# Optimization experiments

Measured on AMD Instinct MI355X. Metric: run time of the kernel, lower is better.

The kernel has to match this reference:

```python
import jax, jax.numpy as jnp
import numpy as np

B, L, D, H = 1, 2048, 1024, 16
d = D // H  # head dim = 64


def setup_inputs() -> dict:
    key = jax.random.key(0)
    ks = jax.random.split(key, 8)
    s = 1.0 / np.sqrt(D)
    return {
        "x": jax.random.normal(ks[0], (B, L, D), jnp.float32),
        "Wqkv_w": (jax.random.normal(ks[1], (D, 3 * D), jnp.float32) * s),
        "Wqkv_b": jnp.zeros((3 * D,), jnp.float32),
        "out_w": (jax.random.normal(ks[2], (D, D), jnp.float32) * s),
        "out_b": jnp.zeros((D,), jnp.float32),
        "W_static": jnp.zeros((H, d, d), jnp.float32),
        "Lambda_raw": jax.random.uniform(ks[3], (H, d, d), jnp.float32, -3.0, 3.0),
        "Gamma": jax.random.uniform(ks[4], (H, d, d), jnp.float32, -0.5 / np.sqrt(d), 0.5 / np.sqrt(d)),
        "gate_w1": (jax.random.normal(ks[5], (D, D // 2), jnp.float32) * s),
        "gate_b1": jnp.zeros((D // 2,), jnp.float32),
        "gate_w2": (jax.random.normal(ks[6], (D // 2, H), jnp.float32) * (1.0 / np.sqrt(D // 2))),
        "gate_b2": jnp.zeros((H,), jnp.float32),
    }


def _forward(x, Wqkv_w, Wqkv_b, out_w, out_b, W_static, Lambda_raw, Gamma,
             gate_w1, gate_b1, gate_w2, gate_b2):
    Bb, Ll, Dm = x.shape
    Hh = Gamma.shape[0]
    dd = Dm // Hh
    scale = 1.0 / np.sqrt(dd)

    # qkv projection: (B,L,3D) -> (3, B, H, L, d) layout
    qkv = (x @ Wqkv_w + Wqkv_b).reshape(Bb, Ll, 3, Hh, dd)
    q = jnp.transpose(qkv[:, :, 0], (0, 2, 1, 3))  # (B,H,L,d)
    k = jnp.transpose(qkv[:, :, 1], (0, 2, 1, 3))
    v = jnp.transpose(qkv[:, :, 2], (0, 2, 1, 3))

    # --- softmax branch (causal, additive -10000 mask like the original) ---
    scores = jnp.einsum('bhid,bhjd->bhij', q, k) * scale
    causal_mask = jnp.triu(jnp.full((Ll, Ll), -10000.0, dtype=scores.dtype), 1)
    attn = jax.nn.softmax(scores + causal_mask, axis=-1)
    y_softmax = jnp.einsum('bhij,bhjd->bhid', attn, v)

    # --- STP branch: linear recurrence over time via lax.scan ---
    retention = 1.0 - jax.nn.sigmoid(Lambda_raw)  # (H,d,d)
    k_stp = k * scale

    def step(state, inp):
        q_t, k_t, v_t = inp  # each (B,H,d)
        hebbian = v_t[..., :, None] * k_t[..., None, :]          # (B,H,d,d)
        state = retention * state + Gamma * hebbian              # (B,H,d,d)
        y_t = jnp.einsum('bhij,bhj->bhi', W_static + state, q_t)  # (B,H,d)
        return state, y_t

    state0 = jnp.zeros((Bb, Hh, dd, dd), x.dtype)
    qT = jnp.moveaxis(q, 2, 0)      # (L,B,H,d)
    kT = jnp.moveaxis(k_stp, 2, 0)
    vT = jnp.moveaxis(v, 2, 0)
    _, ys = jax.lax.scan(step, state0, (qT, kT, vT))
    y_stp = jnp.moveaxis(ys, 0, 2)  # (B,H,L,d)

    # --- learned gate: Linear -> GELU(exact) -> Linear -> sigmoid ---
    g = jax.nn.gelu(x @ gate_w1 + gate_b1, approximate=False)
    alpha = jax.nn.sigmoid(g @ gate_w2 + gate_b2)        # (B,L,H)
    alpha = jnp.transpose(alpha, (0, 2, 1))[..., None]   # (B,H,L,1)

    y = alpha * y_softmax + (1.0 - alpha) * y_stp        # (B,H,L,d)
    y = jnp.transpose(y, (0, 2, 1, 3)).reshape(Bb, Ll, Dm)
    return y @ out_w + out_b


def reference(x, Wqkv_w, Wqkv_b, out_w, out_b, W_static, Lambda_raw, Gamma,
              gate_w1, gate_b1, gate_w2, gate_b2):
    return _forward(x, Wqkv_w, Wqkv_b, out_w, out_b, W_static, Lambda_raw,
                    Gamma, gate_w1, gate_b1, gate_w2, gate_b2)
```

## Files before the change

### kernel.cpp

```cpp
#include <hip/hip_runtime.h>
#include <hip/hip_bf16.h>

#define L_SEQ 2048
#define DMODEL 1024
#define NHEAD 16
#define DHEAD 64
#define D3 3072

typedef __attribute__((ext_vector_type(8))) short s8v;
typedef __attribute__((ext_vector_type(4))) float f4v;
typedef unsigned int u32;
#define AS1 __attribute__((address_space(1)))
#define AS3 __attribute__((address_space(3)))

__device__ __forceinline__ short f2bf(float f) {
  __hip_bfloat16 h = __float2bfloat16(f);
  return *reinterpret_cast<short*>(&h);
}
__device__ __forceinline__ float bf2f(short s) {
  return __uint_as_float(((u32)(unsigned short)s) << 16);
}
__device__ __forceinline__ int pack2bf(float lo, float hi) {
  return (int)(((unsigned)(unsigned short)f2bf(hi) << 16) |
               (unsigned)(unsigned short)f2bf(lo));
}

__device__ __forceinline__ void transpose32(const float* __restrict__ W,
    short* __restrict__ Wt, int K, int N, int bx, int by, int tid)
{
  __shared__ float T[32][33];
  int col = tid & 31, rb = tid >> 5;
  #pragma unroll
  for (int it = 0; it < 4; ++it) {
    int r = it * 8 + rb;
    T[r][col] = W[(size_t)(by * 32 + r) * N + bx * 32 + col];
  }
  __syncthreads();
  #pragma unroll
  for (int it = 0; it < 4; ++it) {
    int r = it * 8 + rb;
    Wt[(size_t)(bx * 32 + r) * K + by * 32 + col] = f2bf(T[col][r]);
  }
}

__global__ __launch_bounds__(256) void prep_kernel(
    const float* __restrict__ x, short* __restrict__ xb,
    const float* __restrict__ Wqkv_w, const float* __restrict__ gw1,
    const float* __restrict__ out_w, short* __restrict__ wt_buf,
    short* __restrict__ wtO)
{
  int b = blockIdx.x, tid = threadIdx.x;
  if (b < 2048) {
    int i = (b * 256 + tid) * 4;
    float4 v = *(const float4*)(x + i);
    short4 o;
    o.x = f2bf(v.x); o.y = f2bf(v.y); o.z = f2bf(v.z); o.w = f2bf(v.w);
    *(short4*)(xb + i) = o;
  } else if (b < 5120) {
    int r = b - 2048;
    transpose32(Wqkv_w, wt_buf, 1024, 3072, r % 96, r / 96, tid);
  } else if (b < 5632) {
    int r = b - 5120;
    transpose32(gw1, wt_buf + 3072 * 1024, 1024, 512, r % 16, r / 16, tid);
  } else {
    int r = b - 5632;
    transpose32(out_w, wtO, 1024, 1024, r % 32, r / 32, tid);
  }
}

template<int BM, int BN, int MODE>
__global__ __launch_bounds__(256, 6) void gemm_mfma(
    const short* __restrict__ A, const short* __restrict__ Bt,
    const float* __restrict__ bias, const float* __restrict__ bias2,
    float* __restrict__ C, short* __restrict__ C2,
    short* __restrict__ QbP, short* __restrict__ KbP,
    int M, int N, int K)
{
  constexpr int LA = BM / 64, LB = BN / 64;
  constexpr int WM = BM / 2, WN = BN / 2;
  constexpr int MT = WM / 16, NT = WN / 16;
  __shared__ __align__(16) short As[2][BM * 32];
  __shared__ __align__(16) short Bs[2][BN * 32];
  const int tid = threadIdx.x;
  const int w = tid >> 6, lane = tid & 63;
  const int quad = lane >> 4, c = lane & 15;
  int n0, kb, ke;
  size_t cofs = 0;
  if (MODE == 3) {
    n0 = (blockIdx.x & 15) * BN;
    int kh = blockIdx.x >> 4;
    kb = kh * (K / 2); ke = kb + K / 2;
    cofs = (size_t)kh * M * N;
  } else {
    n0 = blockIdx.x * BN; kb = 0; ke = K;
  }
  const int m0 = blockIdx.y * BM;
  const int wm = (w & 1) * WM, wn = (w >> 1) * WN;
  f4v acc[MT][NT] = {};

  auto stage = [&](int buf, int k0) {
    #pragma unroll
    for (int it = 0; it < LA; ++it) {
      int off = (it * 256 + tid) * 16;
      int row = off >> 6, colh = (off & 63) >> 1;
      __builtin_amdgcn_global_load_lds(
          (const AS1 u32*)(A + (size_t)(m0 + row) * K + k0 + colh),
          (AS3 u32*)(&As[buf][0] + (off >> 1)), 16, 0, 0);
    }
    #pragma unroll
    for (int it = 0; it < LB; ++it) {
      int off = (it * 256 + tid) * 16;
      int row = off >> 6, colh = (off & 63) >> 1;
      __builtin_amdgcn_global_load_lds(
          (const AS1 u32*)(Bt + (size_t)(n0 + row) * K + k0 + colh),
          (AS3 u32*)(&Bs[buf][0] + (off >> 1)), 16, 0, 0);
    }
  };
  stage(0, kb);
  int cur = 0;
  for (int k0 = kb; k0 < ke; k0 += 32) {
    __syncthreads();
    if (k0 + 32 < ke) stage(cur ^ 1, k0 + 32);
    s8v af[MT], bf[NT];
    #pragma unroll
    for (int mt = 0; mt < MT; ++mt)
      af[mt] = *(s8v*)&As[cur][(wm + mt * 16 + c) * 32 + quad * 8];
    #pragma unroll
    for (int nt = 0; nt < NT; ++nt)
      bf[nt] = *(s8v*)&Bs[cur][(wn + nt * 16 + c) * 32 + quad * 8];
    #pragma unroll
    for (int mt = 0; mt < MT; ++mt)
      #pragma unroll
      for (int nt = 0; nt < NT; ++nt)
        acc[mt][nt] = __builtin_amdgcn_mfma_f32_16x16x32_bf16(
            af[mt], bf[nt], acc[mt][nt], 0, 0, 0);
    cur ^= 1;
  }
  #pragma unroll
  for (int mt = 0; mt < MT; ++mt)
    #pragma unroll
    for (int r = 0; r < 4; ++r) {
      int m = m0 + wm + mt * 16 + quad * 4 + r;
      #pragma unroll
      for (int nt = 0; nt < NT; ++nt) {
        int n = n0 + wn + nt * 16 + c;
        float v = acc[mt][nt][r];
        if (MODE == 3) {
          C[cofs + (size_t)m * N + n] = v;
        } else {
          if (n < 2048) {
            float v2 = v + bias[n];
            int hh = (n >> 6) & 15, ee = n & 63;
            short* dst = (n < 1024) ? QbP : KbP;
            dst[((size_t)hh * 2048 + m) * 64 + ee] = f2bf(v2);
          } else if (n < 3072) {
            C[(size_t)m * 1024 + (n - 2048)] = v + bias[n];
          } else {
            float t = v + bias2[n - 3072];
            t = 0.5f * t * (1.0f + erff(t * 0.70710678118654752f));
            C2[(size_t)m * 512 + (n - 3072)] = f2bf(t);
          }
        }
      }
    }
}

__global__ __launch_bounds__(256) void splitk_add(const float* __restrict__ Cp,
    const float* __restrict__ bias, float* __restrict__ out)
{
  int i = (blockIdx.x * 256 + threadIdx.x) * 4;
  float4 a = *(const float4*)(Cp + i);
  float4 b = *(const float4*)(Cp + 2097152 + i);
  float4 bs = *(const float4*)(bias + (i & 1023));
  float4 o;
  o.x = a.x + b.x + bs.x; o.y = a.y + b.y + bs.y;
  o.z = a.z + b.z + bs.z; o.w = a.w + b.w + bs.w;
  *(float4*)(out + i) = o;
}

__device__ __forceinline__ int piece_slot(int qt, int h, int p) {
  if (qt >= 16) return (qt - 16) * 48 + h * 3 + p;
  if (qt >= 8)  return 768 + (qt - 8) * 32 + h * 2 + p;
  return 1024 + qt * 16 + h;
}

__global__ __launch_bounds__(256) void attn_mfma(
    const short* __restrict__ Qb, const short* __restrict__ Kb,
    const short* __restrict__ Vtb, float* __restrict__ Opart,
    float* __restrict__ mpart, float* __restrict__ lpart)
{
  const int bid = blockIdx.x;
  int h, qt, p, np;
  if (bid < 768)       { int j = bid;        qt = 31 - j / 48; int r = j % 48; h = r / 3; p = r % 3; np = 3; }
  else if (bid < 1024) { int j = bid - 768;  qt = 15 - j / 32; int r = j % 32; h = r >> 1; p = r & 1; np = 2; }
  else                 { int j = bid - 1024; qt = 7 - (j >> 4); h = j & 15; p = 0; np = 1; }
  const int n = qt + 1;
  const int ts = (p * n) / np, te = ((p + 1) * n) / np;
  const int ps = piece_slot(qt, h, p);
  float* Odst = Opart + (size_t)ps * 4096;
  float* mdst = mpart + ps * 64;
  float* ldst = lpart + ps * 64;

  const int q0 = qt * 64;
  const int tid = threadIdx.x;
  const int w = tid >> 6, lane = tid & 63;
  const int quad = lane >> 4, c = lane & 15;

  __shared__ __align__(16) char smem[27648];
  short* Ks = (short*)smem;
  short* Vt = Ks + 4608;
  short* Ps = Vt + 4608;
  float* Ob = (float*)smem;

  const int qrow = q0 + w * 16 + c;
  s8v qf[2];
  qf[0] = *(const s8v*)(Qb + ((size_t)h * 2048 + qrow) * 64 + quad * 8);
  qf[1] = *(const s8v*)(Qb + ((size_t)h * 2048 + qrow) * 64 + 32 + quad * 8);

  const int srow = tid >> 3, sc = (tid & 7) * 8;
  int4 pk0, pk1, pv0, pv1;
  auto load_tile = [&](int t0) {
    const short* kbase = Kb + ((size_t)h * 2048 + t0 * 64) * 64;
    const short* vbase = Vtb + (size_t)h * 64 * 2048 + t0 * 64;
    pk0 = *(const int4*)(kbase + (size_t)srow * 64 + sc);
    pk1 = *(const int4*)(kbase + (size_t)(srow + 32) * 64 + sc);
    pv0 = *(const int4*)(vbase + (size_t)srow * 2048 + sc);
    pv1 = *(const int4*)(vbase + (size_t)(srow + 32) * 2048 + sc);
  };
  load_tile(ts);

  f4v o_acc[4] = {};
  float m = -1e30f, l = 0.f;

  for (int t0 = ts; t0 < te; ++t0) {
    __syncthreads();
    *(int4*)&Ks[srow * 72 + sc] = pk0;
    *(int4*)&Ks[(srow + 32) * 72 + sc] = pk1;
    *(int4*)&Vt[srow * 72 + sc] = pv0;
    *(int4*)&Vt[(srow + 32) * 72 + sc] = pv1;
    __syncthreads();
    if (t0 + 1 < te) load_tile(t0 + 1);

    f4v s_acc[4] = {};
    #pragma unroll
    for (int kt = 0; kt < 4; ++kt) {
      #pragma unroll
      for (int kc = 0; kc < 2; ++kc) {
        s8v kf = *(s8v*)&Ks[(kt * 16 + c) * 72 + kc * 32 + quad * 8];
        s_acc[kt] = __builtin_amdgcn_mfma_f32_16x16x32_bf16(kf, qf[kc], s_acc[kt], 0, 0, 0);
      }
    }
    float sv[4][4];
    bool full = (t0 * 64 + 63) <= (q0 + w * 16);
    #pragma unroll
    for (int kt = 0; kt < 4; ++kt)
      #pragma unroll
      for (int r = 0; r < 4; ++r) {
        float s = s_acc[kt][r] * 0.125f;
        if (!full) {
          int key = t0 * 64 + kt * 16 + quad * 4 + r;
          s = (key <= qrow) ? s : -1e30f;
        }
        sv[kt][r] = s;
      }
    float mloc = -1e30f;
    #pragma unroll
    for (int kt = 0; kt < 4; ++kt)
      #pragma unroll
      for (int r = 0; r < 4; ++r) mloc = fmaxf(mloc, sv[kt][r]);
    mloc = fmaxf(mloc, __shfl_xor(mloc, 16));
    mloc = fmaxf(mloc, __shfl_xor(mloc, 32));
    float mnew = fmaxf(fmaxf(m, mloc), -1e20f);
    float alpha = __expf(m - mnew);
    m = mnew;
    float pv[4][4], ls = 0.f;
    #pragma unroll
    for (int kt = 0; kt < 4; ++kt)
      #pragma unroll
      for (int r = 0; r < 4; ++r) { pv[kt][r] = __expf(sv[kt][r] - mnew); ls += pv[kt][r]; }
    ls += __shfl_xor(ls, 16);
    ls += __shfl_xor(ls, 32);
    l = l * alpha + ls;
    #pragma unroll
    for (int mt = 0; mt < 4; ++mt)
      #pragma unroll
      for (int r = 0; r < 4; ++r) o_acc[mt][r] *= alpha;
    short* Pw = Ps + w * 1152;
    #pragma unroll
    for (int kt = 0; kt < 4; ++kt) {
      *(int*)&Pw[c * 72 + kt * 16 + quad * 4]     = pack2bf(pv[kt][0], pv[kt][1]);
      *(int*)&Pw[c * 72 + kt * 16 + quad * 4 + 2] = pack2bf(pv[kt][2], pv[kt][3]);
    }
    #pragma unroll
    for (int kc2 = 0; kc2 < 2; ++kc2) {
      s8v pf = *(s8v*)&Pw[c * 72 + kc2 * 32 + quad * 8];
      #pragma unroll
      for (int mt = 0; mt < 4; ++mt) {
        s8v vf = *(s8v*)&Vt[(mt * 16 + c) * 72 + kc2 * 32 + quad * 8];
        o_acc[mt] = __builtin_amdgcn_mfma_f32_16x16x32_bf16(vf, pf, o_acc[mt], 0, 0, 0);
      }
    }
  }

  __syncthreads();
  #pragma unroll
  for (int mt = 0; mt < 4; ++mt)
    #pragma unroll
    for (int r = 0; r < 4; ++r)
      Ob[(w * 16 + c) * 66 + mt * 16 + quad * 4 + r] = o_acc[mt][r];
  if (quad == 0) { mdst[w * 16 + c] = m; ldst[w * 16 + c] = l; }
  __syncthreads();
  for (int i = tid; i < 4096; i += 256)
    Odst[i] = Ob[(i >> 6) * 66 + (i & 63)];
}

__global__ __launch_bounds__(256) void attn_merge(
    const float* __restrict__ Opart, const float* __restrict__ mpart,
    const float* __restrict__ lpart, const float* __restrict__ ystp,
    const float* __restrict__ alpha, short* __restrict__ ycb)
{
  int bid = blockIdx.x;
  int h = bid >> 5, qt = bid & 31;
  int np = (qt >= 16) ? 3 : ((qt >= 8) ? 2 : 1);
  int ps0 = piece_slot(qt, h, 0);
  int tid = threadIdx.x;
  for (int it = 0; it < 16; ++it) {
    int idx = it * 256 + tid;
    int q = idx >> 6, e = idx & 63;
    int gq = qt * 64 + q;
    float ms = mpart[ps0 * 64 + q];
    for (int p2 = 1; p2 < np; ++p2)
      ms = fmaxf(ms, mpart[(ps0 + p2) * 64 + q]);
    float oo = 0.f, ll = 0.f;
    for (int p2 = 0; p2 < np; ++p2) {
      float wp = __expf(mpart[(ps0 + p2) * 64 + q] - ms);
      oo += Opart[(size_t)(ps0 + p2) * 4096 + idx] * wp;
      ll += lpart[(ps0 + p2) * 64 + q] * wp;
    }
    float ys = oo / ll;
    float a = alpha[gq * 16 + h];
    float yst = ystp[((size_t)h * 2048 + gq) * 64 + e];
    ycb[(size_t)gq * 1024 + h * 64 + e] = f2bf(a * ys + (1.f - a) * yst);
  }
}

__global__ __launch_bounds__(256) void stp_local(const float* __restrict__ Vf,
    const short* __restrict__ Kb, const float* __restrict__ Lam,
    const float* __restrict__ Gam, float* __restrict__ states,
    short* __restrict__ Vtb)
{
  int c = blockIdx.x, h = blockIdx.y;
  int tid = threadIdx.x;
  int i = tid >> 2, j0 = (tid & 3) * 16;
  __shared__ float Kc[64][64];
  __shared__ float Vc[64][65];
  for (int idx = tid; idx < 1024; idx += 256) {
    int t = idx >> 4, e4 = (idx & 15) * 4;
    short4 ks = *(const short4*)(Kb + ((size_t)h * 2048 + c * 64 + t) * 64 + e4);
    Kc[t][e4]     = bf2f(ks.x) * 0.125f;
    Kc[t][e4 + 1] = bf2f(ks.y) * 0.125f;
    Kc[t][e4 + 2] = bf2f(ks.z) * 0.125f;
    Kc[t][e4 + 3] = bf2f(ks.w) * 0.125f;
    float4 vv = *(const float4*)(Vf + (size_t)(c * 64 + t) * 1024 + h * 64 + e4);
    Vc[t][e4] = vv.x; Vc[t][e4 + 1] = vv.y; Vc[t][e4 + 2] = vv.z; Vc[t][e4 + 3] = vv.w;
  }
  float r[16], g[16], s[16];
  #pragma unroll
  for (int e = 0; e < 16; ++e) {
    int idx = h * 4096 + i * 64 + j0 + e;
    r[e] = 1.f / (1.f + expf(Lam[idx]));
    g[e] = Gam[idx];
    s[e] = 0.f;
  }
  __syncthreads();
  for (int idx = tid; idx < 2048; idx += 256) {
    int dim = idx >> 5, k2 = idx & 31;
    *(int*)&Vtb[((size_t)h * 64 + dim) * 2048 + c * 64 + k2 * 2] =
        pack2bf(Vc[k2 * 2][dim], Vc[k2 * 2 + 1][dim]);
  }
  for (int t = 0; t < 64; ++t) {
    float v = Vc[t][i];
    #pragma unroll
    for (int e = 0; e < 16; ++e)
      s[e] = r[e] * s[e] + g[e] * (v * Kc[t][j0 + e]);
  }
  #pragma unroll
  for (int e = 0; e < 16; ++e)
    states[((size_t)h * 32 + c) * 4096 + i * 64 + j0 + e] = s[e];
}

__global__ __launch_bounds__(256) void stp_scan(const float* __restrict__ Lam,
                                                float* __restrict__ states)
{
  int gid = blockIdx.x * 256 + threadIdx.x;
  float r = 1.f / (1.f + expf(Lam[gid]));
  float r64 = r;
  #pragma unroll
  for (int q = 0; q < 6; ++q) r64 *= r64;
  int h = gid >> 12, low = gid & 4095;
  const size_t base = (size_t)h * 32 * 4096 + low;
  float v[32];
  #pragma unroll
  for (int c = 0; c < 32; ++c) v[c] = states[base + (size_t)c * 4096];
  float acc = 0.f;
  #pragma unroll
  for (int c = 0; c < 32; ++c) {
    float d = v[c];
    v[c] = acc;
    acc = r64 * acc + d;
  }
  #pragma unroll
  for (int c = 0; c < 32; ++c) states[base + (size_t)c * 4096] = v[c];
}

__global__ __launch_bounds__(256) void stp_out(const float* __restrict__ Vf,
    const short* __restrict__ Kb, const short* __restrict__ Qb,
    const float* __restrict__ Lam, const float* __restrict__ Gam,
    const float* __restrict__ Wst, const float* __restrict__ states,
    float* __restrict__ ystp)
{
  int c = blockIdx.x, h = blockIdx.y;
  int tid = threadIdx.x;
  int i = tid >> 2, j0 = (tid & 3) * 16;
  __shared__ float Kc[64][64];
  __shared__ float Vc[64][64];
  __shared__ float Qc[64][64];
  for (int idx = tid; idx < 1024; idx += 256) {
    int t = idx >> 4, e4 = (idx & 15) * 4;
    size_t bo = ((size_t)h * 2048 + c * 64 + t) * 64 + e4;
    short4 ks = *(const short4*)(Kb + bo);
    short4 qs = *(const short4*)(Qb + bo);
    Kc[t][e4]     = bf2f(ks.x) * 0.125f;
    Kc[t][e4 + 1] = bf2f(ks.y) * 0.125f;
    Kc[t][e4 + 2] = bf2f(ks.z) * 0.125f;
    Kc[t][e4 + 3] = bf2f(ks.w) * 0.125f;
    Qc[t][e4]     = bf2f(qs.x);
    Qc[t][e4 + 1] = bf2f(qs.y);
    Qc[t][e4 + 2] = bf2f(qs.z);
    Qc[t][e4 + 3] = bf2f(qs.w);
    float4 vv = *(const float4*)(Vf + (size_t)(c * 64 + t) * 1024 + h * 64 + e4);
    Vc[t][e4] = vv.x; Vc[t][e4 + 1] = vv.y; Vc[t][e4 + 2] = vv.z; Vc[t][e4 + 3] = vv.w;
  }
  float r[16], g[16], s[16], w[16];
  #pragma unroll
  for (int e = 0; e < 16; ++e) {
    int idx = h * 4096 + i * 64 + j0 + e;
    r[e] = 1.f / (1.f + expf(Lam[idx]));
    g[e] = Gam[idx];
    w[e] = Wst[idx];
    s[e] = states[((size_t)h * 32 + c) * 4096 + i * 64 + j0 + e];
  }
  __syncthreads();
  for (int t = 0; t < 64; ++t) {
    float v = Vc[t][i];
    float y = 0.f;
    #pragma unroll
    for (int e = 0; e < 16; ++e) {
      s[e] = r[e] * s[e] + g[e] * (v * Kc[t][j0 + e]);
      y += (w[e] + s[e]) * Qc[t][j0 + e];
    }
    y += __shfl_xor(y, 1);
    y += __shfl_xor(y, 2);
    if ((tid & 3) == 0)
      ystp[((size_t)h * L_SEQ + c * 64 + t) * 64 + i] = y;
  }
}

__global__ __launch_bounds__(256) void gate2_kernel(const short* __restrict__ g_bf,
    const float* __restrict__ w2, const float* __restrict__ b2,
    float* __restrict__ alpha)
{
  int tid = threadIdx.x;
  int gid = blockIdx.x * 16 + (tid >> 4);
  int sub = tid & 15;
  int l = gid >> 4, h = gid & 15;
  const short* grow = g_bf + (size_t)l * 512 + sub * 32;
  float acc = 0.f;
  #pragma unroll
  for (int c2 = 0; c2 < 32; c2 += 2) {
    u32 pk = *(const u32*)(grow + c2);
    float g0 = __uint_as_float(pk << 16);
    float g1 = __uint_as_float(pk & 0xffff0000u);
    int cb = sub * 32 + c2;
    acc += g0 * w2[cb * 16 + h] + g1 * w2[(cb + 1) * 16 + h];
  }
  acc += __shfl_xor(acc, 1);
  acc += __shfl_xor(acc, 2);
  acc += __shfl_xor(acc, 4);
  acc += __shfl_xor(acc, 8);
  if (sub == 0) alpha[gid] = 1.f / (1.f + expf(-(acc + b2[h])));
}

extern "C" void kernel_launch(void* const* d_in, const int* in_sizes, int n_in,
                              void* d_out, int out_size, void* d_ws, size_t ws_size,
                              hipStream_t stream) {
  (void)in_sizes; (void)n_in; (void)out_size; (void)ws_size;
  const float* x      = (const float*)d_in[0];
  const float* Wqkv_w = (const float*)d_in[1];
  const float* Wqkv_b = (const float*)d_in[2];
  const float* out_w  = (const float*)d_in[3];
  const float* out_b  = (const float*)d_in[4];
  const float* W_st   = (const float*)d_in[5];
  const float* Lam    = (const float*)d_in[6];
  const float* Gam    = (const float*)d_in[7];
  const float* gw1    = (const float*)d_in[8];
  const float* gb1    = (const float*)d_in[9];
  const float* gw2    = (const float*)d_in[10];
  const float* gb2    = (const float*)d_in[11];

  float* ws     = (float*)d_ws;
  float* Vf     = ws;
  float* ystp   = ws + 2097152;
  float* states = ws + 4194304;
  short* xb     = (short*)(ws + 6291456);
  short* wt_buf = (short*)(ws + 7340032);
  short* g_bf   = (short*)(ws + 9175040);
  float* alpha  = ws + 9699328;
  short* Qb     = (short*)(ws + 9732096);
  short* Kb     = (short*)(ws + 10780672);
  short* wtO    = (short*)(ws + 11829248);
  short* Vtb    = (short*)(ws + 12353536);
  short* ycb    = (short*)(ws + 13402112);
  float* Opart  = ws + 14450688;
  float* mpart  = ws + 19169280;
  float* lpart  = ws + 19243008;
  float* Cpart  = ws + 19316736;

  prep_kernel<<<dim3(6656), 256, 0, stream>>>(x, xb, Wqkv_w, gw1, out_w, wt_buf, wtO);
  gemm_mfma<64, 64, 2><<<dim3(56, 32), 256, 0, stream>>>(
      xb, wt_buf, Wqkv_b, gb1, Vf, g_bf, Qb, Kb, 2048, 3584, 1024);
  gate2_kernel<<<dim3(2048), 256, 0, stream>>>(g_bf, gw2, gb2, alpha);
  stp_local<<<dim3(32, 16), 256, 0, stream>>>(Vf, Kb, Lam, Gam, states, Vtb);
  stp_scan<<<dim3(256), 256, 0, stream>>>(Lam, states);
  stp_out<<<dim3(32, 16), 256, 0, stream>>>(Vf, Kb, Qb, Lam, Gam, W_st, states, ystp);
  attn_mfma<<<dim3(1152), 256, 0, stream>>>(Qb, Kb, Vtb, Opart, mpart, lpart);
  attn_merge<<<dim3(512), 256, 0, stream>>>(Opart, mpart, lpart, ystp, alpha, ycb);
  gemm_mfma<64, 64, 3><<<dim3(32, 32), 256, 0, stream>>>(
      ycb, wtO, nullptr, nullptr, Cpart, nullptr, nullptr, nullptr, 2048, 1024, 1024);
  splitk_add<<<dim3(2048), 256, 0, stream>>>(Cpart, out_b, (float*)d_out);
}
```

Before: 286.7 us.

## Drop split-K output GEMM, coarsen attention splits, widen STP blocks

The output projection no longer uses split-K with a separate reduction kernel. It now writes the bias-added result directly, which removes one launch and the partial-sum traffic. Attention work splitting is reduced from 3/2/1 pieces per query tile to 2/1 (768 blocks instead of 1152), cutting merge overhead in exchange for less parallelism on long rows. The STP local/out kernels now use 512 threads with 8 state columns per thread, halving per-thread serial work and register use at the cost of an extra shuffle.

New measurement: 281.8 us. No clear change (-1.7%).

```diff
diff --git a/kernel.cpp b/kernel.cpp
--- a/kernel.cpp
+++ b/kernel.cpp
@@ -84,17 +84,7 @@
   const int tid = threadIdx.x;
   const int w = tid >> 6, lane = tid & 63;
   const int quad = lane >> 4, c = lane & 15;
-  int n0, kb, ke;
-  size_t cofs = 0;
-  if (MODE == 3) {
-    n0 = (blockIdx.x & 15) * BN;
-    int kh = blockIdx.x >> 4;
-    kb = kh * (K / 2); ke = kb + K / 2;
-    cofs = (size_t)kh * M * N;
-  } else {
-    n0 = blockIdx.x * BN; kb = 0; ke = K;
-  }
-  const int m0 = blockIdx.y * BM;
+  const int m0 = blockIdx.y * BM, n0 = blockIdx.x * BN;
   const int wm = (w & 1) * WM, wn = (w >> 1) * WN;
   f4v acc[MT][NT] = {};
 
@@ -116,11 +106,11 @@
           (AS3 u32*)(&Bs[buf][0] + (off >> 1)), 16, 0, 0);
     }
   };
-  stage(0, kb);
+  stage(0, 0);
   int cur = 0;
-  for (int k0 = kb; k0 < ke; k0 += 32) {
+  for (int k0 = 0; k0 < K; k0 += 32) {
     __syncthreads();
-    if (k0 + 32 < ke) stage(cur ^ 1, k0 + 32);
+    if (k0 + 32 < K) stage(cur ^ 1, k0 + 32);
     s8v af[MT], bf[NT];
     #pragma unroll
     for (int mt = 0; mt < MT; ++mt)
@@ -145,8 +135,8 @@
       for (int nt = 0; nt < NT; ++nt) {
         int n = n0 + wn + nt * 16 + c;
         float v = acc[mt][nt][r];
-        if (MODE == 3) {
-          C[cofs + (size_t)m * N + n] = v;
+        if (MODE == 0) {
+          C[(size_t)m * N + n] = v + bias[n];
         } else {
           if (n < 2048) {
             float v2 = v + bias[n];
@@ -165,23 +155,9 @@
     }
 }
 
-__global__ __launch_bounds__(256) void splitk_add(const float* __restrict__ Cp,
-    const float* __restrict__ bias, float* __restrict__ out)
-{
-  int i = (blockIdx.x * 256 + threadIdx.x) * 4;
-  float4 a = *(const float4*)(Cp + i);
-  float4 b = *(const float4*)(Cp + 2097152 + i);
-  float4 bs = *(const float4*)(bias + (i & 1023));
-  float4 o;
-  o.x = a.x + b.x + bs.x; o.y = a.y + b.y + bs.y;
-  o.z = a.z + b.z + bs.z; o.w = a.w + b.w + bs.w;
-  *(float4*)(out + i) = o;
-}
-
 __device__ __forceinline__ int piece_slot(int qt, int h, int p) {
-  if (qt >= 16) return (qt - 16) * 48 + h * 3 + p;
-  if (qt >= 8)  return 768 + (qt - 8) * 32 + h * 2 + p;
-  return 1024 + qt * 16 + h;
+  if (qt >= 16) return (qt - 16) * 32 + h * 2 + p;
+  return 512 + qt * 16 + h;
 }
 
 __global__ __launch_bounds__(256) void attn_mfma(
@@ -190,12 +166,16 @@
     float* __restrict__ mpart, float* __restrict__ lpart)
 {
   const int bid = blockIdx.x;
-  int h, qt, p, np;
-  if (bid < 768)       { int j = bid;        qt = 31 - j / 48; int r = j % 48; h = r / 3; p = r % 3; np = 3; }
-  else if (bid < 1024) { int j = bid - 768;  qt = 15 - j / 32; int r = j % 32; h = r >> 1; p = r & 1; np = 2; }
-  else                 { int j = bid - 1024; qt = 7 - (j >> 4); h = j & 15; p = 0; np = 1; }
-  const int n = qt + 1;
-  const int ts = (p * n) / np, te = ((p + 1) * n) / np;
+  int h, qt, p, ts, te;
+  if (bid < 512) {
+    qt = 31 - (bid >> 5);
+    int r = bid & 31; h = r >> 1; p = r & 1;
+    int n = qt + 1, n2 = (n + 1) >> 1;
+    ts = p ? n2 : 0; te = p ? n : n2;
+  } else {
+    int j = bid - 512; qt = 15 - (j >> 4); h = j & 15; p = 0;
+    ts = 0; te = qt + 1;
+  }
   const int ps = piece_slot(qt, h, p);
   float* Odst = Opart + (size_t)ps * 4096;
   float* mdst = mpart + ps * 64;
@@ -321,7 +301,7 @@
 {
   int bid = blockIdx.x;
   int h = bid >> 5, qt = bid & 31;
-  int np = (qt >= 16) ? 3 : ((qt >= 8) ? 2 : 1);
+  int np = (qt >= 16) ? 2 : 1;
   int ps0 = piece_slot(qt, h, 0);
   int tid = threadIdx.x;
   for (int it = 0; it < 16; ++it) {
@@ -344,17 +324,17 @@
   }
 }
 
-__global__ __launch_bounds__(256) void stp_local(const float* __restrict__ Vf,
+__global__ __launch_bounds__(512) void stp_local(const float* __restrict__ Vf,
     const short* __restrict__ Kb, const float* __restrict__ Lam,
     const float* __restrict__ Gam, float* __restrict__ states,
     short* __restrict__ Vtb)
 {
   int c = blockIdx.x, h = blockIdx.y;
   int tid = threadIdx.x;
-  int i = tid >> 2, j0 = (tid & 3) * 16;
+  int i = tid >> 3, j0 = (tid & 7) * 8;
   __shared__ float Kc[64][64];
   __shared__ float Vc[64][65];
-  for (int idx = tid; idx < 1024; idx += 256) {
+  for (int idx = tid; idx < 1024; idx += 512) {
     int t = idx >> 4, e4 = (idx & 15) * 4;
     short4 ks = *(const short4*)(Kb + ((size_t)h * 2048 + c * 64 + t) * 64 + e4);
     Kc[t][e4]     = bf2f(ks.x) * 0.125f;
@@ -364,16 +344,16 @@
     float4 vv = *(const float4*)(Vf + (size_t)(c * 64 + t) * 1024 + h * 64 + e4);
     Vc[t][e4] = vv.x; Vc[t][e4 + 1] = vv.y; Vc[t][e4 + 2] = vv.z; Vc[t][e4 + 3] = vv.w;
   }
-  float r[16], g[16], s[16];
-  #pragma unroll
-  for (int e = 0; e < 16; ++e) {
+  float r[8], g[8], s[8];
+  #pragma unroll
+  for (int e = 0; e < 8; ++e) {
     int idx = h * 4096 + i * 64 + j0 + e;
     r[e] = 1.f / (1.f + expf(Lam[idx]));
     g[e] = Gam[idx];
     s[e] = 0.f;
   }
   __syncthreads();
-  for (int idx = tid; idx < 2048; idx += 256) {
+  for (int idx = tid; idx < 2048; idx += 512) {
     int dim = idx >> 5, k2 = idx & 31;
     *(int*)&Vtb[((size_t)h * 64 + dim) * 2048 + c * 64 + k2 * 2] =
         pack2bf(Vc[k2 * 2][dim], Vc[k2 * 2 + 1][dim]);
@@ -381,11 +361,11 @@
   for (int t = 0; t < 64; ++t) {
     float v = Vc[t][i];
     #pragma unroll
-    for (int e = 0; e < 16; ++e)
+    for (int e = 0; e < 8; ++e)
       s[e] = r[e] * s[e] + g[e] * (v * Kc[t][j0 + e]);
   }
   #pragma unroll
-  for (int e = 0; e < 16; ++e)
+  for (int e = 0; e < 8; ++e)
     states[((size_t)h * 32 + c) * 4096 + i * 64 + j0 + e] = s[e];
 }
 
@@ -413,7 +393,7 @@
   for (int c = 0; c < 32; ++c) states[base + (size_t)c * 4096] = v[c];
 }
 
-__global__ __launch_bounds__(256) void stp_out(const float* __restrict__ Vf,
+__global__ __launch_bounds__(512) void stp_out(const float* __restrict__ Vf,
     const short* __restrict__ Kb, const short* __restrict__ Qb,
     const float* __restrict__ Lam, const float* __restrict__ Gam,
     const float* __restrict__ Wst, const float* __restrict__ states,
@@ -421,11 +401,11 @@
 {
   int c = blockIdx.x, h = blockIdx.y;
   int tid = threadIdx.x;
-  int i = tid >> 2, j0 = (tid & 3) * 16;
+  int i = tid >> 3, j0 = (tid & 7) * 8;
   __shared__ float Kc[64][64];
   __shared__ float Vc[64][64];
   __shared__ float Qc[64][64];
-  for (int idx = tid; idx < 1024; idx += 256) {
+  for (int idx = tid; idx < 1024; idx += 512) {
     int t = idx >> 4, e4 = (idx & 15) * 4;
     size_t bo = ((size_t)h * 2048 + c * 64 + t) * 64 + e4;
     short4 ks = *(const short4*)(Kb + bo);
@@ -441,9 +421,9 @@
     float4 vv = *(const float4*)(Vf + (size_t)(c * 64 + t) * 1024 + h * 64 + e4);
     Vc[t][e4] = vv.x; Vc[t][e4 + 1] = vv.y; Vc[t][e4 + 2] = vv.z; Vc[t][e4 + 3] = vv.w;
   }
-  float r[16], g[16], s[16], w[16];
-  #pragma unroll
-  for (int e = 0; e < 16; ++e) {
+  float r[8], g[8], s[8], w[8];
+  #pragma unroll
+  for (int e = 0; e < 8; ++e) {
     int idx = h * 4096 + i * 64 + j0 + e;
     r[e] = 1.f / (1.f + expf(Lam[idx]));
     g[e] = Gam[idx];
@@ -455,13 +435,14 @@
     float v = Vc[t][i];
     float y = 0.f;
     #pragma unroll
-    for (int e = 0; e < 16; ++e) {
+    for (int e = 0; e < 8; ++e) {
       s[e] = r[e] * s[e] + g[e] * (v * Kc[t][j0 + e]);
       y += (w[e] + s[e]) * Qc[t][j0 + e];
     }
     y += __shfl_xor(y, 1);
     y += __shfl_xor(y, 2);
-    if ((tid & 3) == 0)
+    y += __shfl_xor(y, 4);
+    if ((tid & 7) == 0)
       ystp[((size_t)h * L_SEQ + c * 64 + t) * 64 + i] = y;
   }
 }
@@ -522,20 +503,18 @@
   short* Vtb    = (short*)(ws + 12353536);
   short* ycb    = (short*)(ws + 13402112);
   float* Opart  = ws + 14450688;
-  float* mpart  = ws + 19169280;
-  float* lpart  = ws + 19243008;
-  float* Cpart  = ws + 19316736;
+  float* mpart  = ws + 17596416;
+  float* lpart  = ws + 17645568;
 
   prep_kernel<<<dim3(6656), 256, 0, stream>>>(x, xb, Wqkv_w, gw1, out_w, wt_buf, wtO);
   gemm_mfma<64, 64, 2><<<dim3(56, 32), 256, 0, stream>>>(
       xb, wt_buf, Wqkv_b, gb1, Vf, g_bf, Qb, Kb, 2048, 3584, 1024);
   gate2_kernel<<<dim3(2048), 256, 0, stream>>>(g_bf, gw2, gb2, alpha);
-  stp_local<<<dim3(32, 16), 256, 0, stream>>>(Vf, Kb, Lam, Gam, states, Vtb);
+  stp_local<<<dim3(32, 16), 512, 0, stream>>>(Vf, Kb, Lam, Gam, states, Vtb);
   stp_scan<<<dim3(256), 256, 0, stream>>>(Lam, states);
-  stp_out<<<dim3(32, 16), 256, 0, stream>>>(Vf, Kb, Qb, Lam, Gam, W_st, states, ystp);
-  attn_mfma<<<dim3(1152), 256, 0, stream>>>(Qb, Kb, Vtb, Opart, mpart, lpart);
+  stp_out<<<dim3(32, 16), 512, 0, stream>>>(Vf, Kb, Qb, Lam, Gam, W_st, states, ystp);
+  attn_mfma<<<dim3(768), 256, 0, stream>>>(Qb, Kb, Vtb, Opart, mpart, lpart);
   attn_merge<<<dim3(512), 256, 0, stream>>>(Opart, mpart, lpart, ystp, alpha, ycb);
-  gemm_mfma<64, 64, 3><<<dim3(32, 32), 256, 0, stream>>>(
-      ycb, wtO, nullptr, nullptr, Cpart, nullptr, nullptr, nullptr, 2048, 1024, 1024);
-  splitk_add<<<dim3(2048), 256, 0, stream>>>(Cpart, out_b, (float*)d_out);
-}
+  gemm_mfma<64, 64, 0><<<dim3(16, 32), 256, 0, stream>>>(
+      ycb, wtO, out_b, nullptr, (float*)d_out, nullptr, nullptr, nullptr, 2048, 1024, 1024);
+}
```
